# Performance work log

Hardware: AMD Instinct MI355X
Metric: run time of the kernel (lower is better)

The kernel has to match this reference:

```python
import jax, jax.numpy as jnp
import numpy as np

D_MODEL = 768
N_HEADS = 12
HEAD_DIM = D_MODEL // N_HEADS
D_FF = 4 * D_MODEL
EPS = 1e-5


def setup_inputs() -> dict:
    key = jax.random.key(0)
    ks = jax.random.split(key, 16)
    s = 0.02
    x = jax.random.normal(ks[0], (2, 2048, D_MODEL), dtype=jnp.float32)
    wq = jax.random.normal(ks[1], (D_MODEL, D_MODEL), dtype=jnp.float32) * s
    bq = jnp.zeros((D_MODEL,), jnp.float32)
    wk = jax.random.normal(ks[2], (D_MODEL, D_MODEL), dtype=jnp.float32) * s
    bk = jnp.zeros((D_MODEL,), jnp.float32)
    wv = jax.random.normal(ks[3], (D_MODEL, D_MODEL), dtype=jnp.float32) * s
    bv = jnp.zeros((D_MODEL,), jnp.float32)
    wo = jax.random.normal(ks[4], (D_MODEL, D_MODEL), dtype=jnp.float32) * s
    bo = jnp.zeros((D_MODEL,), jnp.float32)
    w1 = jax.random.normal(ks[5], (D_MODEL, D_FF), dtype=jnp.float32) * s
    b1 = jnp.zeros((D_FF,), jnp.float32)
    w2 = jax.random.normal(ks[6], (D_FF, D_MODEL), dtype=jnp.float32) * s
    b2 = jnp.zeros((D_MODEL,), jnp.float32)
    ln1_g = jnp.ones((D_MODEL,), jnp.float32)
    ln1_b = jnp.zeros((D_MODEL,), jnp.float32)
    ln2_g = jnp.ones((D_MODEL,), jnp.float32)
    ln2_b = jnp.zeros((D_MODEL,), jnp.float32)
    return dict(x=x, wq=wq, bq=bq, wk=wk, bk=bk, wv=wv, bv=bv, wo=wo, bo=bo,
                w1=w1, b1=b1, w2=w2, b2=b2,
                ln1_g=ln1_g, ln1_b=ln1_b, ln2_g=ln2_g, ln2_b=ln2_b)


def _layernorm(x, g, b):
    mu = jnp.mean(x, axis=-1, keepdims=True)
    var = jnp.mean(jnp.square(x - mu), axis=-1, keepdims=True)
    return (x - mu) * jax.lax.rsqrt(var + EPS) * g + b


def _attention(x, wq, bq, wk, bk, wv, bv, wo, bo):
    B, S, D = x.shape
    def split_heads(t):  # [B,S,D] -> [B,H,S,Hd]
        return t.reshape(B, S, N_HEADS, HEAD_DIM).transpose(0, 2, 1, 3)
    q = split_heads(x @ wq + bq)
    k = split_heads(x @ wk + bk)
    v = split_heads(x @ wv + bv)
    scores = jnp.einsum('bhqd,bhkd->bhqk', q, k) / np.sqrt(HEAD_DIM).astype(np.float32)
    causal = jnp.tril(jnp.ones((S, S), dtype=bool))
    scores = jnp.where(causal, scores, -jnp.inf)
    weights = jax.nn.softmax(scores, axis=-1)
    attn = jnp.einsum('bhqk,bhkd->bhqd', weights, v)
    attn = attn.transpose(0, 2, 1, 3).reshape(B, S, D)
    return attn @ wo + bo


def reference(x, wq, bq, wk, bk, wv, bv, wo, bo, w1, b1, w2, b2,
              ln1_g, ln1_b, ln2_g, ln2_b):
    x = x + _attention(_layernorm(x, ln1_g, ln1_b), wq, bq, wk, bk, wv, bv, wo, bo)
    h = _layernorm(x, ln2_g, ln2_b)
    ff = jax.nn.relu(h @ w1 + b1) @ w2 + b2
    return x + ff
```

## Files before the change

### kernel.cpp

```cpp
#include <hip/hip_runtime.h>
#include <stdint.h>

typedef __bf16 bf16;
typedef float f32x4 __attribute__((ext_vector_type(4)));
typedef bf16 bf16x8 __attribute__((ext_vector_type(8)));
typedef bf16 bf16x4 __attribute__((ext_vector_type(4)));

#define MFMA16(a, b, c) __builtin_amdgcn_mfma_f32_16x16x32_bf16((a), (b), (c), 0, 0, 0)

static __device__ __forceinline__ void load_lds16(const bf16* g, bf16* l) {
  __builtin_amdgcn_global_load_lds(
      (const __attribute__((address_space(1))) void*)g,
      (__attribute__((address_space(3))) void*)l, 16, 0, 0);
}

static __device__ __forceinline__ void xcd_swz(int& bx, int& by, int& bz) {
  int gx = gridDim.x, gy = gridDim.y;
  int lin = blockIdx.x + gx * (blockIdx.y + gy * blockIdx.z);
  int nwg = gx * gy * gridDim.z;
  int nl = (lin & 7) * (nwg >> 3) + (lin >> 3);
  bx = nl % gx;
  int t = nl / gx;
  by = t % gy;
  bz = t / gy;
}

__global__ void __launch_bounds__(256) k_prep(
    const float* __restrict__ x, const float* __restrict__ ln1g,
    const float* __restrict__ ln1b, bf16* __restrict__ h1,
    const float* s0, const float* s1, const float* s2, const float* s3,
    const float* s4, const float* s5,
    bf16* d0, bf16* d1, bf16* d2, bf16* d3, bf16* d4, bf16* d5) {
  int t = blockIdx.x;
  int tid = threadIdx.x;
  if (t < 6912) {
    const float* src; bf16* dst; int R, C;
    if (t < 2304) {
      int z = t / 576; t -= z * 576;
      src = (z == 0) ? s0 : (z == 1) ? s1 : (z == 2) ? s2 : s3;
      dst = (z == 0) ? d0 : (z == 1) ? d1 : (z == 2) ? d2 : d3;
      R = 768; C = 768;
    } else if (t < 4608) {
      t -= 2304; src = s4; dst = d4; R = 768; C = 3072;
    } else {
      t -= 4608; src = s5; dst = d5; R = 3072; C = 768;
    }
    int tcn = C >> 5;
    int tr = t / tcn, tc = t % tcn;
    __shared__ float tile[32][33];
    int tx = tid & 31, ty = tid >> 5;
    for (int i = 0; i < 4; i++)
      tile[ty + i * 8][tx] = src[(size_t)(tr * 32 + ty + i * 8) * C + tc * 32 + tx];
    __syncthreads();
    for (int i = 0; i < 4; i++)
      dst[(size_t)(tc * 32 + ty + i * 8) * R + tr * 32 + tx] = (bf16)tile[tx][ty + i * 8];
  } else {
    int row = t - 6912;
    const float* rp = x + (size_t)row * 768;
    float v0 = rp[tid], v1 = rp[tid + 256], v2 = rp[tid + 512];
    float s = v0 + v1 + v2, sq = v0 * v0 + v1 * v1 + v2 * v2;
    for (int off = 1; off < 64; off <<= 1) {
      s += __shfl_xor(s, off, 64);
      sq += __shfl_xor(sq, off, 64);
    }
    __shared__ float ps[8];
    if ((tid & 63) == 0) { ps[tid >> 6] = s; ps[4 + (tid >> 6)] = sq; }
    __syncthreads();
    s = ps[0] + ps[1] + ps[2] + ps[3];
    sq = ps[4] + ps[5] + ps[6] + ps[7];
    float mu = s * (1.0f / 768.0f);
    float rstd = rsqrtf(sq * (1.0f / 768.0f) - mu * mu + 1e-5f);
    bf16* op = h1 + (size_t)row * 768;
    op[tid] = (bf16)((v0 - mu) * rstd * ln1g[tid] + ln1b[tid]);
    op[tid + 256] = (bf16)((v1 - mu) * rstd * ln1g[tid + 256] + ln1b[tid + 256]);
    op[tid + 512] = (bf16)((v2 - mu) * rstd * ln1g[tid + 512] + ln1b[tid + 512]);
  }
}

__global__ void __launch_bounds__(256) k_ln2_reduce(
    const float* __restrict__ p0, const float* __restrict__ p1,
    const float* __restrict__ x, const float* __restrict__ bo,
    const float* __restrict__ gam, const float* __restrict__ bet,
    float* __restrict__ x1, bf16* __restrict__ h2) {
  int row = blockIdx.x, tid = threadIdx.x;
  size_t base = (size_t)row * 768;
  float v0 = p0[base + tid] + p1[base + tid] + x[base + tid] + bo[tid];
  float v1 = p0[base + tid + 256] + p1[base + tid + 256] + x[base + tid + 256] + bo[tid + 256];
  float v2 = p0[base + tid + 512] + p1[base + tid + 512] + x[base + tid + 512] + bo[tid + 512];
  x1[base + tid] = v0; x1[base + tid + 256] = v1; x1[base + tid + 512] = v2;
  float s = v0 + v1 + v2, sq = v0 * v0 + v1 * v1 + v2 * v2;
  for (int off = 1; off < 64; off <<= 1) {
    s += __shfl_xor(s, off, 64);
    sq += __shfl_xor(sq, off, 64);
  }
  __shared__ float ps[8];
  if ((tid & 63) == 0) { ps[tid >> 6] = s; ps[4 + (tid >> 6)] = sq; }
  __syncthreads();
  s = ps[0] + ps[1] + ps[2] + ps[3];
  sq = ps[4] + ps[5] + ps[6] + ps[7];
  float mu = s * (1.0f / 768.0f);
  float rstd = rsqrtf(sq * (1.0f / 768.0f) - mu * mu + 1e-5f);
  bf16* op = h2 + base;
  op[tid] = (bf16)((v0 - mu) * rstd * gam[tid] + bet[tid]);
  op[tid + 256] = (bf16)((v1 - mu) * rstd * gam[tid + 256] + bet[tid + 256]);
  op[tid + 512] = (bf16)((v2 - mu) * rstd * gam[tid + 512] + bet[tid + 512]);
}

__global__ void __launch_bounds__(256) k_ff2_reduce(
    const float* __restrict__ f0, const float* __restrict__ f1,
    const float* __restrict__ f2, const float* __restrict__ f3,
    const float* __restrict__ x1, const float* __restrict__ b2,
    float* __restrict__ out) {
  size_t i = ((size_t)blockIdx.x * 256 + threadIdx.x) * 4;
  int col = (int)(i % 768);
  f32x4 v = *(const f32x4*)(x1 + i);
  f32x4 b = *(const f32x4*)(b2 + col);
  f32x4 a0 = *(const f32x4*)(f0 + i), a1 = *(const f32x4*)(f1 + i);
  f32x4 a2 = *(const f32x4*)(f2 + i), a3 = *(const f32x4*)(f3 + i);
  *(f32x4*)(out + i) = v + b + a0 + a1 + a2 + a3;
}

template <int MT>
static __device__ __forceinline__ void gemm_core(
    const bf16* __restrict__ A, int lda, const bf16* __restrict__ Bt, int ldb,
    int Kc, int m0, int n0, bf16* As, bf16* Bs, f32x4 acc[MT][4]) {
  int tid = threadIdx.x, w = tid >> 6, lane = tid & 63, quad = lane >> 4, l15 = lane & 15;
  int wr = w >> 1, wc = w & 1;
  int srow = lane >> 2;
  int sk = (((lane & 3) ^ ((srow >> 1) & 3)) * 8);
  int rsw = ((l15 >> 1) & 3);
  const int ABUF = MT * 32 * 32;
  const int BBUF = 128 * 32;

  auto stage = [&](int k0, int buf) {
    bf16* Ab = As + buf * ABUF;
    bf16* Bb = Bs + buf * BBUF;
    if (MT == 4) {
      for (int c = 0; c < 2; c++) {
        int seg = w * 2 + c;
        load_lds16(A + (size_t)(m0 + seg * 16 + srow) * lda + k0 + sk, Ab + seg * 512);
      }
    } else {
      load_lds16(A + (size_t)(m0 + w * 16 + srow) * lda + k0 + sk, Ab + w * 512);
    }
    for (int c = 0; c < 2; c++) {
      int seg = w * 2 + c;
      load_lds16(Bt + (size_t)(n0 + seg * 16 + srow) * ldb + k0 + sk, Bb + seg * 512);
    }
  };

  stage(0, 0);
  stage(32, 1);
  int cur = 0;
  for (int k0 = 0; k0 < Kc; k0 += 32) {
    if (k0 + 32 < Kc) {
      if (MT == 4) asm volatile("s_waitcnt vmcnt(4)" ::: "memory");
      else         asm volatile("s_waitcnt vmcnt(3)" ::: "memory");
    } else {
      asm volatile("s_waitcnt vmcnt(0)" ::: "memory");
    }
    __builtin_amdgcn_s_barrier();
    __builtin_amdgcn_sched_barrier(0);
    if (k0 + 64 < Kc) {
      int nb = cur + 2; if (nb >= 3) nb -= 3;
      stage(k0 + 64, nb);
    }
    const bf16* Ab = As + cur * ABUF;
    const bf16* Bb = Bs + cur * BBUF;
    bf16x8 af[MT], bfr[4];
    for (int mi = 0; mi < MT; mi++)
      af[mi] = *(const bf16x8*)(Ab + (wr * (MT * 16) + mi * 16 + l15) * 32 + ((quad ^ rsw) * 8));
    for (int ni = 0; ni < 4; ni++)
      bfr[ni] = *(const bf16x8*)(Bb + (wc * 64 + ni * 16 + l15) * 32 + ((quad ^ rsw) * 8));
    for (int mi = 0; mi < MT; mi++)
      for (int ni = 0; ni < 4; ni++)
        acc[mi][ni] = MFMA16(af[mi], bfr[ni], acc[mi][ni]);
    cur = cur + 1; if (cur >= 3) cur -= 3;
  }
}

template <int MT>
__global__ void __launch_bounds__(256, MT == 2 ? 4 : 3) k_gemm(
    const bf16* __restrict__ A, const bf16* __restrict__ Bt,
    const float* __restrict__ bias, bf16* __restrict__ outp, int K_, int N_) {
  __shared__ __align__(16) bf16 As[3 * MT * 32 * 32];
  __shared__ __align__(16) bf16 Bs[3 * 128 * 32];
  int bx, by, bz;
  xcd_swz(bx, by, bz);
  int m0 = by * (MT * 32), n0 = bx * 128;
  f32x4 acc[MT][4] = {};
  gemm_core<MT>(A, K_, Bt, K_, K_, m0, n0, As, Bs, acc);
  int tid = threadIdx.x, w = tid >> 6, lane = tid & 63, quad = lane >> 4, l15 = lane & 15;
  int wr = w >> 1, wc = w & 1;
  float bv[4];
  for (int ni = 0; ni < 4; ni++) bv[ni] = bias[n0 + wc * 64 + ni * 16 + l15];
  for (int mi = 0; mi < MT; mi++) {
    int mb = m0 + wr * (MT * 16) + mi * 16 + quad * 4;
    for (int ni = 0; ni < 4; ni++) {
      int n = n0 + wc * 64 + ni * 16 + l15;
      for (int r = 0; r < 4; r++) {
        float val = acc[mi][ni][r] + bv[ni];
        outp[(size_t)(mb + r) * N_ + n] = (bf16)fmaxf(val, 0.0f);
      }
    }
  }
}

template <int MT>
__global__ void __launch_bounds__(256, MT == 2 ? 4 : 3) k_gemm_split(
    const bf16* __restrict__ A, const bf16* __restrict__ Bt,
    float* __restrict__ f0, float* __restrict__ f1,
    float* __restrict__ f2, float* __restrict__ f3, int K_, int Kc, int N_) {
  __shared__ __align__(16) bf16 As[3 * MT * 32 * 32];
  __shared__ __align__(16) bf16 Bs[3 * 128 * 32];
  int bx, by, bz;
  xcd_swz(bx, by, bz);
  int z = bz;
  float* outp = (z == 0) ? f0 : (z == 1) ? f1 : (z == 2) ? f2 : f3;
  int m0 = by * (MT * 32), n0 = bx * 128;
  f32x4 acc[MT][4] = {};
  gemm_core<MT>(A + (size_t)z * Kc, K_, Bt + (size_t)z * Kc, K_, Kc, m0, n0, As, Bs, acc);
  int tid = threadIdx.x, w = tid >> 6, lane = tid & 63, quad = lane >> 4, l15 = lane & 15;
  int wr = w >> 1, wc = w & 1;
  for (int mi = 0; mi < MT; mi++) {
    int mb = m0 + wr * (MT * 16) + mi * 16 + quad * 4;
    for (int ni = 0; ni < 4; ni++) {
      int n = n0 + wc * 64 + ni * 16 + l15;
      for (int r = 0; r < 4; r++)
        outp[(size_t)(mb + r) * N_ + n] = acc[mi][ni][r];
    }
  }
}

template <int MT>
__global__ void __launch_bounds__(256, MT == 2 ? 4 : 3) k_gemm_qkv(
    const bf16* __restrict__ h1, const bf16* __restrict__ wqT,
    const bf16* __restrict__ wkT, const bf16* __restrict__ wvT,
    const float* __restrict__ bq, const float* __restrict__ bk,
    const float* __restrict__ bv, bf16* __restrict__ qb,
    bf16* __restrict__ kb, bf16* __restrict__ vtb) {
  __shared__ __align__(16) bf16 As[3 * MT * 32 * 32];
  __shared__ __align__(16) bf16 Bs[3 * 128 * 32];
  int bx, by, bz;
  xcd_swz(bx, by, bz);
  int z = bz;
  const bf16* Bt = (z == 0) ? wqT : (z == 1) ? wkT : wvT;
  const float* bias = (z == 0) ? bq : (z == 1) ? bk : bv;
  int m0 = by * (MT * 32), n0 = bx * 128;
  f32x4 acc[MT][4] = {};
  gemm_core<MT>(h1, 768, Bt, 768, 768, m0, n0, As, Bs, acc);
  int tid = threadIdx.x, w = tid >> 6, lane = tid & 63, quad = lane >> 4, l15 = lane & 15;
  int wr = w >> 1, wc = w & 1;
  float bvv[4];
  for (int ni = 0; ni < 4; ni++) bvv[ni] = bias[n0 + wc * 64 + ni * 16 + l15];
  for (int mi = 0; mi < MT; mi++) {
    int mb = m0 + wr * (MT * 16) + mi * 16 + quad * 4;
    int b = mb >> 11, s0_ = mb & 2047;
    for (int ni = 0; ni < 4; ni++) {
      int n = n0 + wc * 64 + ni * 16 + l15;
      int h = n >> 6, hd = n & 63;
      if (z < 2) {
        bf16* outp = (z == 0) ? qb : kb;
        size_t base = (size_t)(b * 12 + h) * 2048 * 64;
        for (int r = 0; r < 4; r++)
          outp[base + (size_t)(s0_ + r) * 64 + hd] = (bf16)(acc[mi][ni][r] + bvv[ni]);
      } else {
        bf16x4 pk;
        for (int r = 0; r < 4; r++) pk[r] = (bf16)(acc[mi][ni][r] + bvv[ni]);
        *(bf16x4*)(vtb + (((size_t)(b * 12 + h) * 64 + hd) * 2048 + s0_)) = pk;
      }
    }
  }
}

__global__ void __launch_bounds__(256, 2) k_attn(
    const bf16* __restrict__ qb, const bf16* __restrict__ kb,
    const bf16* __restrict__ vtb, bf16* __restrict__ out) {
  __shared__ __align__(16) bf16 Ks[2 * 128 * 64];
  __shared__ __align__(16) bf16 Vs[2 * 64 * 128];
  __shared__ __align__(16) bf16 Ps[4][16 * 128];
  int qt = 31 - (blockIdx.x / 24);
  int bh = blockIdx.x % 24;
  int q0 = qt * 64;
  int tid = threadIdx.x, w = tid >> 6, lane = tid & 63, quad = lane >> 4, l15 = lane & 15;
  const bf16* qbase = qb + (size_t)bh * 2048 * 64;
  const bf16* kbase = kb + (size_t)bh * 2048 * 64;
  const bf16* vbase = vtb + (size_t)bh * 64 * 2048;

  bf16x8 qf[2];
  for (int ds = 0; ds < 2; ds++)
    qf[ds] = *(const bf16x8*)(qbase + (size_t)(q0 + w * 16 + l15) * 64 + ds * 32 + quad * 8);

  bf16 one_ = (bf16)1.0f;
  bf16x8 ones8 = {one_, one_, one_, one_, one_, one_, one_, one_};

  f32x4 o[4] = {};
  f32x4 lacc = {};

  auto stageKV = [&](int k0, int buf) {
    int rsub = lane >> 3, c8 = lane & 7;
    bf16* Kb = Ks + buf * (128 * 64);
    for (int c = 0; c < 4; c++) {
      int seg = c * 4 + w;
      int row = seg * 8 + rsub;
      load_lds16(kbase + (size_t)(k0 + row) * 64 + ((c8 ^ (row & 7)) * 8), Kb + seg * 512);
    }
    int rsub2 = lane >> 4, c16 = lane & 15;
    bf16* Vb = Vs + buf * (64 * 128);
    for (int c = 0; c < 4; c++) {
      int seg = c * 4 + w;
      int row = seg * 4 + rsub2;
      load_lds16(vbase + (size_t)row * 2048 + k0 + ((c16 ^ (row & 15)) * 8), Vb + seg * 512);
    }
  };

  const float C2 = 0.18033688011112042f;
  int nkt = (qt >> 1) + 1;
  stageKV(0, 0);
  int cur = 0;
  for (int kt = 0; kt < nkt; kt++) {
    int k0 = kt * 128;
    __syncthreads();
    if (kt + 1 < nkt) stageKV(k0 + 128, cur ^ 1);
    const bf16* Kb = Ks + cur * (128 * 64);
    const bf16* Vb = Vs + cur * (64 * 128);

    f32x4 sc[8] = {};
    __builtin_amdgcn_s_setprio(1);
    for (int kj = 0; kj < 8; kj++) {
      int krow = kj * 16 + l15;
      for (int ds = 0; ds < 2; ds++) {
        bf16x8 kf = *(const bf16x8*)(Kb + krow * 64 + (((ds * 4 + quad) ^ (krow & 7)) * 8));
        sc[kj] = MFMA16(qf[ds], kf, sc[kj]);
      }
    }
    __builtin_amdgcn_s_setprio(0);
    if (kt == nkt - 1) {
      int qg = q0 + w * 16 + quad * 4;
      for (int kj = 0; kj < 8; kj++) {
        int kg = k0 + kj * 16 + l15;
        for (int r = 0; r < 4; r++)
          if (kg > qg + r) sc[kj][r] = -3.0e38f;
      }
    }
    for (int kj = 0; kj < 8; kj++)
      for (int r = 0; r < 4; r++)
        sc[kj][r] = exp2f(sc[kj][r] * C2);
    for (int kj = 0; kj < 8; kj++) {
      int colb = kj * 16 + l15;
      int chb = colb >> 3, cin = colb & 7;
      for (int r = 0; r < 4; r++) {
        int prow = quad * 4 + r;
        Ps[w][prow * 128 + ((chb ^ prow) * 8) + cin] = (bf16)sc[kj][r];
      }
    }
    __builtin_amdgcn_s_setprio(1);
    for (int ks = 0; ks < 4; ks++) {
      int prow = l15;
      bf16x8 pf = *(const bf16x8*)(&Ps[w][prow * 128 + (((ks * 4 + quad) ^ prow) * 8)]);
      lacc = MFMA16(pf, ones8, lacc);
      for (int dj = 0; dj < 4; dj++) {
        int vrow = dj * 16 + l15;
        bf16x8 vf = *(const bf16x8*)(Vb + vrow * 128 + (((ks * 4 + quad) ^ (vrow & 15)) * 8));
        o[dj] = MFMA16(pf, vf, o[dj]);
      }
    }
    __builtin_amdgcn_s_setprio(0);
    cur ^= 1;
  }
  int b = bh / 12, h = bh % 12;
  f32x4 rl;
  for (int r = 0; r < 4; r++) rl[r] = 1.0f / lacc[r];
  int srow = q0 + w * 16 + quad * 4;
  for (int dj = 0; dj < 4; dj++) {
    int d = h * 64 + dj * 16 + l15;
    for (int r = 0; r < 4; r++)
      out[(size_t)(b * 2048 + srow + r) * 768 + d] = (bf16)(o[dj][r] * rl[r]);
  }
}

extern "C" void kernel_launch(void* const* d_in, const int* in_sizes, int n_in,
                              void* d_out, int out_size, void* d_ws, size_t ws_size,
                              hipStream_t stream) {
  const float* x    = (const float*)d_in[0];
  const float* wq   = (const float*)d_in[1];
  const float* bq   = (const float*)d_in[2];
  const float* wk   = (const float*)d_in[3];
  const float* bk   = (const float*)d_in[4];
  const float* wv   = (const float*)d_in[5];
  const float* bv   = (const float*)d_in[6];
  const float* wo   = (const float*)d_in[7];
  const float* bo   = (const float*)d_in[8];
  const float* w1   = (const float*)d_in[9];
  const float* b1   = (const float*)d_in[10];
  const float* w2   = (const float*)d_in[11];
  const float* b2   = (const float*)d_in[12];
  const float* ln1g = (const float*)d_in[13];
  const float* ln1b = (const float*)d_in[14];
  const float* ln2g = (const float*)d_in[15];
  const float* ln2b = (const float*)d_in[16];

  char* p = (char*)d_ws;
  bf16* wqT = (bf16*)p; p += (size_t)768 * 768 * 2;
  bf16* wkT = (bf16*)p; p += (size_t)768 * 768 * 2;
  bf16* wvT = (bf16*)p; p += (size_t)768 * 768 * 2;
  bf16* woT = (bf16*)p; p += (size_t)768 * 768 * 2;
  bf16* w1T = (bf16*)p; p += (size_t)768 * 3072 * 2;
  bf16* w2T = (bf16*)p; p += (size_t)768 * 3072 * 2;
  bf16* h1   = (bf16*)p; p += (size_t)4096 * 768 * 2;
  bf16* qbuf = (bf16*)p; p += (size_t)4096 * 768 * 2;
  bf16* kbuf = (bf16*)p; p += (size_t)4096 * 768 * 2;
  bf16* vtb  = (bf16*)p; p += (size_t)4096 * 768 * 2;
  bf16* att  = (bf16*)p; p += (size_t)4096 * 768 * 2;
  float* x1  = (float*)p; p += (size_t)4096 * 768 * 4;
  bf16* h2   = (bf16*)p; p += (size_t)4096 * 768 * 2;
  bf16* ffm  = (bf16*)p; p += (size_t)4096 * 3072 * 2;
  float* p0  = (float*)p; p += (size_t)4096 * 768 * 4;
  float* p1  = (float*)p; p += (size_t)4096 * 768 * 4;
  float* f0 = (float*)h1;
  float* f1 = (float*)kbuf;
  float* f2 = p0;
  float* f3 = p1;

  k_prep<<<dim3(11008), dim3(256), 0, stream>>>(
      x, ln1g, ln1b, h1, wq, wk, wv, wo, w1, w2, wqT, wkT, wvT, woT, w1T, w2T);
  k_gemm_qkv<2><<<dim3(6, 64, 3), dim3(256), 0, stream>>>(
      h1, wqT, wkT, wvT, bq, bk, bv, qbuf, kbuf, vtb);
  k_attn<<<dim3(768), dim3(256), 0, stream>>>(qbuf, kbuf, vtb, att);
  k_gemm_split<2><<<dim3(6, 64, 2), dim3(256), 0, stream>>>(
      att, woT, p0, p1, p0, p1, 768, 384, 768);
  k_ln2_reduce<<<dim3(4096), dim3(256), 0, stream>>>(
      p0, p1, x, bo, ln2g, ln2b, x1, h2);
  k_gemm<4><<<dim3(24, 32), dim3(256), 0, stream>>>(
      h2, w1T, b1, ffm, 768, 3072);
  k_gemm_split<4><<<dim3(6, 32, 4), dim3(256), 0, stream>>>(
      ffm, w2T, f0, f1, f2, f3, 3072, 768, 768);
  k_ff2_reduce<<<dim3(3072), dim3(256), 0, stream>>>(
      f0, f1, f2, f3, x1, b2, (float*)d_out);
}
```

Baseline: 277.4 us.

## Use 64-wide K double-buffered GEMM core and halve FF2 split-K partials

Adds a GEMM core that stages two 32-wide K sub-tiles per step (K step of 64) with double buffering and one barrier per 64 K, and uses it for the QKV, out-projection and FF2 GEMMs. FF2 changes from split-K 4 with 128-row tiles to split-K 2 with 64-row tiles, so the final reduce reads two fp32 partial buffers instead of four. The aim is fewer barriers per K, less partial-sum traffic and a different grid shape for FF2. In exchange, prefetch depth drops from three buffers to two, each block uses more LDS, and the launch bound changes from 4 to 3 blocks per CU, which may reduce occupancy.

```diff
diff --git a/kernel.cpp b/kernel.cpp
--- a/kernel.cpp
+++ b/kernel.cpp
@@ -108,7 +108,6 @@
 
 __global__ void __launch_bounds__(256) k_ff2_reduce(
     const float* __restrict__ f0, const float* __restrict__ f1,
-    const float* __restrict__ f2, const float* __restrict__ f3,
     const float* __restrict__ x1, const float* __restrict__ b2,
     float* __restrict__ out) {
   size_t i = ((size_t)blockIdx.x * 256 + threadIdx.x) * 4;
@@ -116,8 +115,7 @@
   f32x4 v = *(const f32x4*)(x1 + i);
   f32x4 b = *(const f32x4*)(b2 + col);
   f32x4 a0 = *(const f32x4*)(f0 + i), a1 = *(const f32x4*)(f1 + i);
-  f32x4 a2 = *(const f32x4*)(f2 + i), a3 = *(const f32x4*)(f3 + i);
-  *(f32x4*)(out + i) = v + b + a0 + a1 + a2 + a3;
+  *(f32x4*)(out + i) = v + b + a0 + a1;
 }
 
 template <int MT>
@@ -180,7 +178,66 @@
 }
 
 template <int MT>
-__global__ void __launch_bounds__(256, MT == 2 ? 4 : 3) k_gemm(
+static __device__ __forceinline__ void gemm_core64(
+    const bf16* __restrict__ A, int lda, const bf16* __restrict__ Bt, int ldb,
+    int Kc, int m0, int n0, bf16* As, bf16* Bs, f32x4 acc[MT][4]) {
+  int tid = threadIdx.x, w = tid >> 6, lane = tid & 63, quad = lane >> 4, l15 = lane & 15;
+  int wr = w >> 1, wc = w & 1;
+  int srow = lane >> 2;
+  int sk = (((lane & 3) ^ ((srow >> 1) & 3)) * 8);
+  int rsw = ((l15 >> 1) & 3);
+  const int ASUB = MT * 32 * 32;
+  const int BSUB = 128 * 32;
+  const int ABUF = 2 * ASUB;
+  const int BBUF = 2 * BSUB;
+
+  auto stage = [&](int k0, int buf) {
+    bf16* Ab = As + buf * ABUF;
+    bf16* Bb = Bs + buf * BBUF;
+    for (int h = 0; h < 2; h++) {
+      if (MT == 4) {
+        for (int c = 0; c < 2; c++) {
+          int seg = w * 2 + c;
+          load_lds16(A + (size_t)(m0 + seg * 16 + srow) * lda + k0 + h * 32 + sk,
+                     Ab + h * ASUB + seg * 512);
+        }
+      } else {
+        load_lds16(A + (size_t)(m0 + w * 16 + srow) * lda + k0 + h * 32 + sk,
+                   Ab + h * ASUB + w * 512);
+      }
+      for (int c = 0; c < 2; c++) {
+        int seg = w * 2 + c;
+        load_lds16(Bt + (size_t)(n0 + seg * 16 + srow) * ldb + k0 + h * 32 + sk,
+                   Bb + h * BSUB + seg * 512);
+      }
+    }
+  };
+
+  stage(0, 0);
+  int cur = 0;
+  for (int k0 = 0; k0 < Kc; k0 += 64) {
+    __syncthreads();
+    if (k0 + 64 < Kc) stage(k0 + 64, cur ^ 1);
+    const bf16* Ab = As + cur * ABUF;
+    const bf16* Bb = Bs + cur * BBUF;
+    for (int h = 0; h < 2; h++) {
+      bf16x8 af[MT], bfr[4];
+      for (int mi = 0; mi < MT; mi++)
+        af[mi] = *(const bf16x8*)(Ab + h * ASUB +
+                 (wr * (MT * 16) + mi * 16 + l15) * 32 + ((quad ^ rsw) * 8));
+      for (int ni = 0; ni < 4; ni++)
+        bfr[ni] = *(const bf16x8*)(Bb + h * BSUB +
+                  (wc * 64 + ni * 16 + l15) * 32 + ((quad ^ rsw) * 8));
+      for (int mi = 0; mi < MT; mi++)
+        for (int ni = 0; ni < 4; ni++)
+          acc[mi][ni] = MFMA16(af[mi], bfr[ni], acc[mi][ni]);
+    }
+    cur ^= 1;
+  }
+}
+
+template <int MT>
+__global__ void __launch_bounds__(256, 3) k_gemm(
     const bf16* __restrict__ A, const bf16* __restrict__ Bt,
     const float* __restrict__ bias, bf16* __restrict__ outp, int K_, int N_) {
   __shared__ __align__(16) bf16 As[3 * MT * 32 * 32];
@@ -206,24 +263,21 @@
   }
 }
 
-template <int MT>
-__global__ void __launch_bounds__(256, MT == 2 ? 4 : 3) k_gemm_split(
+__global__ void __launch_bounds__(256, 3) k_gemm_split64(
     const bf16* __restrict__ A, const bf16* __restrict__ Bt,
-    float* __restrict__ f0, float* __restrict__ f1,
-    float* __restrict__ f2, float* __restrict__ f3, int K_, int Kc, int N_) {
-  __shared__ __align__(16) bf16 As[3 * MT * 32 * 32];
-  __shared__ __align__(16) bf16 Bs[3 * 128 * 32];
+    float* __restrict__ f0, float* __restrict__ f1, int K_, int Kc, int N_) {
+  __shared__ __align__(16) bf16 As[2 * 2 * 2 * 32 * 32];
+  __shared__ __align__(16) bf16 Bs[2 * 2 * 128 * 32];
   int bx, by, bz;
   xcd_swz(bx, by, bz);
-  int z = bz;
-  float* outp = (z == 0) ? f0 : (z == 1) ? f1 : (z == 2) ? f2 : f3;
-  int m0 = by * (MT * 32), n0 = bx * 128;
-  f32x4 acc[MT][4] = {};
-  gemm_core<MT>(A + (size_t)z * Kc, K_, Bt + (size_t)z * Kc, K_, Kc, m0, n0, As, Bs, acc);
+  float* outp = (bz == 0) ? f0 : f1;
+  int m0 = by * 64, n0 = bx * 128;
+  f32x4 acc[2][4] = {};
+  gemm_core64<2>(A + (size_t)bz * Kc, K_, Bt + (size_t)bz * Kc, K_, Kc, m0, n0, As, Bs, acc);
   int tid = threadIdx.x, w = tid >> 6, lane = tid & 63, quad = lane >> 4, l15 = lane & 15;
   int wr = w >> 1, wc = w & 1;
-  for (int mi = 0; mi < MT; mi++) {
-    int mb = m0 + wr * (MT * 16) + mi * 16 + quad * 4;
+  for (int mi = 0; mi < 2; mi++) {
+    int mb = m0 + wr * 32 + mi * 16 + quad * 4;
     for (int ni = 0; ni < 4; ni++) {
       int n = n0 + wc * 64 + ni * 16 + l15;
       for (int r = 0; r < 4; r++)
@@ -232,29 +286,28 @@
   }
 }
 
-template <int MT>
-__global__ void __launch_bounds__(256, MT == 2 ? 4 : 3) k_gemm_qkv(
+__global__ void __launch_bounds__(256, 3) k_gemm_qkv64(
     const bf16* __restrict__ h1, const bf16* __restrict__ wqT,
     const bf16* __restrict__ wkT, const bf16* __restrict__ wvT,
     const float* __restrict__ bq, const float* __restrict__ bk,
     const float* __restrict__ bv, bf16* __restrict__ qb,
     bf16* __restrict__ kb, bf16* __restrict__ vtb) {
-  __shared__ __align__(16) bf16 As[3 * MT * 32 * 32];
-  __shared__ __align__(16) bf16 Bs[3 * 128 * 32];
+  __shared__ __align__(16) bf16 As[2 * 2 * 2 * 32 * 32];
+  __shared__ __align__(16) bf16 Bs[2 * 2 * 128 * 32];
   int bx, by, bz;
   xcd_swz(bx, by, bz);
   int z = bz;
   const bf16* Bt = (z == 0) ? wqT : (z == 1) ? wkT : wvT;
   const float* bias = (z == 0) ? bq : (z == 1) ? bk : bv;
-  int m0 = by * (MT * 32), n0 = bx * 128;
-  f32x4 acc[MT][4] = {};
-  gemm_core<MT>(h1, 768, Bt, 768, 768, m0, n0, As, Bs, acc);
+  int m0 = by * 64, n0 = bx * 128;
+  f32x4 acc[2][4] = {};
+  gemm_core64<2>(h1, 768, Bt, 768, 768, m0, n0, As, Bs, acc);
   int tid = threadIdx.x, w = tid >> 6, lane = tid & 63, quad = lane >> 4, l15 = lane & 15;
   int wr = w >> 1, wc = w & 1;
   float bvv[4];
   for (int ni = 0; ni < 4; ni++) bvv[ni] = bias[n0 + wc * 64 + ni * 16 + l15];
-  for (int mi = 0; mi < MT; mi++) {
-    int mb = m0 + wr * (MT * 16) + mi * 16 + quad * 4;
+  for (int mi = 0; mi < 2; mi++) {
+    int mb = m0 + wr * 32 + mi * 16 + quad * 4;
     int b = mb >> 11, s0_ = mb & 2047;
     for (int ni = 0; ni < 4; ni++) {
       int n = n0 + wc * 64 + ni * 16 + l15;
@@ -419,22 +472,20 @@
   float* p1  = (float*)p; p += (size_t)4096 * 768 * 4;
   float* f0 = (float*)h1;
   float* f1 = (float*)kbuf;
-  float* f2 = p0;
-  float* f3 = p1;
 
   k_prep<<<dim3(11008), dim3(256), 0, stream>>>(
       x, ln1g, ln1b, h1, wq, wk, wv, wo, w1, w2, wqT, wkT, wvT, woT, w1T, w2T);
-  k_gemm_qkv<2><<<dim3(6, 64, 3), dim3(256), 0, stream>>>(
+  k_gemm_qkv64<<<dim3(6, 64, 3), dim3(256), 0, stream>>>(
       h1, wqT, wkT, wvT, bq, bk, bv, qbuf, kbuf, vtb);
   k_attn<<<dim3(768), dim3(256), 0, stream>>>(qbuf, kbuf, vtb, att);
-  k_gemm_split<2><<<dim3(6, 64, 2), dim3(256), 0, stream>>>(
-      att, woT, p0, p1, p0, p1, 768, 384, 768);
+  k_gemm_split64<<<dim3(6, 64, 2), dim3(256), 0, stream>>>(
+      att, woT, p0, p1, 768, 384, 768);
   k_ln2_reduce<<<dim3(4096), dim3(256), 0, stream>>>(
       p0, p1, x, bo, ln2g, ln2b, x1, h2);
   k_gemm<4><<<dim3(24, 32), dim3(256), 0, stream>>>(
       h2, w1T, b1, ffm, 768, 3072);
-  k_gemm_split<4><<<dim3(6, 32, 4), dim3(256), 0, stream>>>(
-      ffm, w2T, f0, f1, f2, f3, 3072, 768, 768);
+  k_gemm_split64<<<dim3(6, 64, 2), dim3(256), 0, stream>>>(
+      ffm, w2T, f0, f1, 3072, 1536, 768);
   k_ff2_reduce<<<dim3(3072), dim3(256), 0, stream>>>(
-      f0, f1, f2, f3, x1, b2, (float*)d_out);
-}
+      f0, f1, x1, b2, (float*)d_out);
+}
```

New measurement: 265.8 us. 1.04x faster.
